# Performance work log

Measured on AMD Instinct MI355X. Metric: run time of the kernel, lower is better.

Reference implementation:

```python
import jax, jax.numpy as jnp
import numpy as np

N_NODES = 50000
N_EDGES = 1600000
IN_FEAT = 256
HIDDEN = 128
N_CLASSES = 16


def gcn_conv(x, edge_index, W, b, n_nodes):
    """PyG GCNConv: x' = D^{-1/2} (A+I) D^{-1/2} (x @ W) + b."""
    h = x @ W  # project first (PyG order), messages are in out_dim
    src, dst = edge_index[0], edge_index[1]
    loops = jnp.arange(n_nodes, dtype=src.dtype)
    src = jnp.concatenate([src, loops])
    dst = jnp.concatenate([dst, loops])
    # degree of A+I (count incoming edges incl. self loop)
    deg = jax.ops.segment_sum(jnp.ones_like(dst, dtype=h.dtype), dst, num_segments=n_nodes)
    dis = jax.lax.rsqrt(deg)  # deg >= 1 thanks to self loops
    norm = dis[src] * dis[dst]  # [E+N]
    msgs = h[src] * norm[:, None]  # gather + scale
    out = jax.ops.segment_sum(msgs, dst, num_segments=n_nodes)  # scatter-add
    return out + b


def setup_inputs() -> dict:
    key = jax.random.key(0)
    k_x, k_e, k_w1, k_b1, k_w2, k_b2 = jax.random.split(key, 6)
    x = jax.random.normal(k_x, (N_NODES, IN_FEAT), dtype=jnp.float32)
    edge_index = jax.random.randint(k_e, (2, N_EDGES), 0, N_NODES, dtype=jnp.int64)
    s1 = 1.0 / np.sqrt(IN_FEAT)
    s2 = 1.0 / np.sqrt(HIDDEN)
    W1 = jax.random.uniform(k_w1, (IN_FEAT, HIDDEN), jnp.float32, -s1, s1)
    b1 = jax.random.uniform(k_b1, (HIDDEN,), jnp.float32, -s1, s1)
    W2 = jax.random.uniform(k_w2, (HIDDEN, N_CLASSES), jnp.float32, -s2, s2)
    b2 = jax.random.uniform(k_b2, (N_CLASSES,), jnp.float32, -s2, s2)
    return {"x": x, "edge_index": edge_index, "W1": W1, "b1": b1, "W2": W2, "b2": b2}


def reference(x, edge_index, W1, b1, W2, b2):
    n = x.shape[0]
    h = gcn_conv(x, edge_index, W1, b1, n)
    h = jax.nn.relu(h)
    logits = gcn_conv(h, edge_index, W2, b2, n)
    return logits, jax.nn.softmax(logits, axis=1)
```

## Files before the change

### kernel.cpp

```cpp
#include <hip/hip_runtime.h>
#include <hip/hip_bf16.h>
#include <math.h>

#define N_NODES 50000
#define N_EDGES 1600000
#define IN_FEAT 256
#define HIDDEN 128
#define N_CLASSES 16

#define ECHUNK 8192
#define NCHK 196
#define NBKT 196
#define BCAP 10240

typedef __attribute__((ext_vector_type(8))) short short8;
typedef __attribute__((ext_vector_type(4))) float floatx4;

__device__ __forceinline__ unsigned short f2bf(float f) {
    unsigned u = __float_as_uint(f);
    return (unsigned short)((u + 0x7fffu + ((u >> 16) & 1u)) >> 16);
}

__device__ __forceinline__ unsigned pk2bf(float a, float b) {
    __hip_bfloat162 h = __float22bfloat162_rn(make_float2(a, b));
    union { __hip_bfloat162 h; unsigned u; } cv;
    cv.h = h;
    return cv.u;
}

__device__ __forceinline__ float bflo(unsigned u) { return __uint_as_float(u << 16); }
__device__ __forceinline__ float bfhi(unsigned u) { return __uint_as_float(u & 0xffff0000u); }

__global__ __launch_bounds__(256) void scatter_edges2(const int* __restrict__ src,
                                                      const int* __restrict__ dst,
                                                      int* __restrict__ cursor,
                                                      unsigned int* __restrict__ sorted,
                                                      const float* __restrict__ W1,
                                                      unsigned short* __restrict__ w1t) {
    __shared__ int hloc[256];
    int t = threadIdx.x;
    hloc[t] = 0;
    if (blockIdx.x < HIDDEN)
        w1t[blockIdx.x * IN_FEAT + t] = f2bf(W1[t * HIDDEN + blockIdx.x]);
    __syncthreads();
    int base = blockIdx.x * ECHUNK;
    int end = min(base + ECHUNK, N_EDGES);
    for (int i = base + t; i < end; i += 256)
        atomicAdd(&hloc[dst[i] >> 8], 1);
    __syncthreads();
    int cnt = hloc[t];
    int lbase = t * BCAP + atomicAdd(&cursor[t], cnt);
    __syncthreads();
    hloc[t] = lbase;
    __syncthreads();
    for (int i = base + t; i < end; i += 256) {
        int d = dst[i];
        int s = src[i];
        int pos = atomicAdd(&hloc[d >> 8], 1);
        sorted[pos] = ((unsigned)d << 16) | (unsigned)s;
    }
}

__global__ __launch_bounds__(256) void build_csr2(const unsigned int* __restrict__ sorted,
                                                  const int* __restrict__ cursor,
                                                  int* __restrict__ rs,
                                                  int* __restrict__ re,
                                                  float* __restrict__ dis,
                                                  unsigned short* __restrict__ csr_src) {
    __shared__ int cnt[256];
    __shared__ int roff[256];
    int t = threadIdx.x;
    int bkt = blockIdx.x;
    int ebase = bkt * BCAP;
    int eend = ebase + cursor[bkt];
    cnt[t] = 0;
    __syncthreads();
    for (int i = ebase + t; i < eend; i += 256)
        atomicAdd(&cnt[(sorted[i] >> 16) & 255], 1);
    __syncthreads();
    int v = cnt[t];
    roff[t] = v;
    __syncthreads();
    for (int off = 1; off < 256; off <<= 1) {
        int x = (t >= off) ? roff[t - off] : 0;
        __syncthreads();
        roff[t] += x;
        __syncthreads();
    }
    int excl = roff[t] - v;
    int node = bkt * 256 + t;
    if (node < N_NODES) {
        rs[node] = ebase + excl;
        re[node] = ebase + excl + v;
        dis[node] = 1.0f / sqrtf((float)(v + 1));
    }
    __syncthreads();
    cnt[t] = ebase + excl;
    __syncthreads();
    for (int i = ebase + t; i < eend; i += 256) {
        unsigned e = sorted[i];
        int pos = atomicAdd(&cnt[(e >> 16) & 255], 1);
        csr_src[pos] = (unsigned short)(e & 0xffffu);
    }
}

#define XCH 260

__global__ __launch_bounds__(256) void gemm1_mfma(const float* __restrict__ x,
                                                  const unsigned short* __restrict__ w1t,
                                                  const float* __restrict__ dis,
                                                  unsigned int* __restrict__ g1) {
    __shared__ float xs[2][8 * XCH];
    int tid = threadIdx.x;
    int w = tid >> 6;
    int lane = tid & 63;
    int quad = lane >> 4;
    int c = lane & 15;
    int row_base = blockIdx.x * 64;
    int wrow = (w >> 1) * 32;
    int col_base = (w & 1) * 64;

    int st_row = min(row_base + 16 * w + (lane >> 3), N_NODES - 1);
    int st_row2 = min(row_base + 16 * w + 8 + (lane >> 3), N_NODES - 1);
    const float* gp1 = x + (size_t)st_row * IN_FEAT + (lane & 7) * 4;
    const float* gp2 = x + (size_t)st_row2 * IN_FEAT + (lane & 7) * 4;

    floatx4 acc[2][4] = {};
    const unsigned short* bp[4];
#pragma unroll
    for (int nt = 0; nt < 4; ++nt)
        bp[nt] = w1t + (size_t)(col_base + nt * 16 + c) * IN_FEAT + quad * 8;

    int dwoff[2];
#pragma unroll
    for (int rt = 0; rt < 2; ++rt) {
        int rit = wrow + rt * 16 + c;
        dwoff[rt] = (rit >> 3) * XCH + (rit & 7) * 32 + quad * 8;
    }

#define STAGE(buf, k0)                                                                  \
    do {                                                                                \
        __builtin_amdgcn_global_load_lds(                                               \
            (const __attribute__((address_space(1))) void*)(gp1 + (k0)),                \
            (__attribute__((address_space(3))) void*)&xs[buf][(2 * w) * XCH], 16, 0, 0);\
        __builtin_amdgcn_global_load_lds(                                               \
            (const __attribute__((address_space(1))) void*)(gp2 + (k0)),                \
            (__attribute__((address_space(3))) void*)&xs[buf][(2 * w + 1) * XCH], 16, 0, 0);\
    } while (0)

    STAGE(0, 0);
    __syncthreads();

    int buf = 0;
#pragma unroll
    for (int kk = 0; kk < 8; ++kk) {
        if (kk < 7) STAGE(buf ^ 1, (kk + 1) * 32);
        short8 b[4];
#pragma unroll
        for (int nt = 0; nt < 4; ++nt)
            b[nt] = *(const short8*)(bp[nt] + kk * 32);
        short8 a[2];
#pragma unroll
        for (int rt = 0; rt < 2; ++rt) {
            float4 f0 = *(const float4*)&xs[buf][dwoff[rt]];
            float4 f1 = *(const float4*)&xs[buf][dwoff[rt] + 4];
            union { short8 s; unsigned u[4]; } au;
            au.u[0] = pk2bf(f0.x, f0.y);
            au.u[1] = pk2bf(f0.z, f0.w);
            au.u[2] = pk2bf(f1.x, f1.y);
            au.u[3] = pk2bf(f1.z, f1.w);
            a[rt] = au.s;
        }
#pragma unroll
        for (int rt = 0; rt < 2; ++rt)
#pragma unroll
            for (int nt = 0; nt < 4; ++nt)
                acc[rt][nt] = __builtin_amdgcn_mfma_f32_16x16x32_bf16(a[rt], b[nt], acc[rt][nt], 0, 0, 0);
        __syncthreads();
        buf ^= 1;
    }
#undef STAGE

    bool evenlane = (lane & 1) == 0;
#pragma unroll
    for (int rt = 0; rt < 2; ++rt) {
#pragma unroll
        for (int reg = 0; reg < 4; ++reg) {
            int row = row_base + wrow + rt * 16 + quad * 4 + reg;
            float dv = dis[min(row, N_NODES - 1)];
#pragma unroll
            for (int nt = 0; nt < 4; ++nt) {
                float v = acc[rt][nt][reg] * dv;
                float vo = __shfl_xor(v, 1);
                if (evenlane && row < N_NODES) {
                    unsigned pkd = (unsigned)f2bf(v) | ((unsigned)f2bf(vo) << 16);
                    g1[(size_t)row * 64 + (col_base >> 1) + nt * 8 + (c >> 1)] = pkd;
                }
            }
        }
    }
}

__global__ __launch_bounds__(256) void agg1_gemm2(const unsigned int* __restrict__ g1,
                                                  const int* __restrict__ rs,
                                                  const int* __restrict__ re,
                                                  const unsigned short* __restrict__ csr_src,
                                                  const float* __restrict__ dis,
                                                  const float* __restrict__ b1,
                                                  const float* __restrict__ W2,
                                                  float* __restrict__ g2) {
    __shared__ float w2s[HIDDEN * N_CLASSES];
    __shared__ float rsh[4][HIDDEN];
    int tid = threadIdx.x;
    for (int i = tid; i < HIDDEN * N_CLASSES; i += 256) w2s[i] = W2[i];
    __syncthreads();

    int wave = tid >> 6;
    int lane = tid & 63;
    int hi = lane >> 5;
    int m = lane & 31;
    int node = blockIdx.x * 4 + wave;
    const uint2* g = (const uint2*)g1;

    float s0 = 0.f, s1 = 0.f, s2 = 0.f, s3 = 0.f;
    float t0 = 0.f, t1 = 0.f, t2 = 0.f, t3 = 0.f;
    if (hi == 0) {
        uint2 su = g[(size_t)node * 32 + m];
        s0 = bflo(su.x); s1 = bfhi(su.x); s2 = bflo(su.y); s3 = bfhi(su.y);
    }

    int e0 = rs[node], e1 = re[node];
    int e = e0;
    for (; e + 16 <= e1; e += 16) {
        int i0 = csr_src[e + 0 + hi], i1 = csr_src[e + 2 + hi];
        int i2 = csr_src[e + 4 + hi], i3 = csr_src[e + 6 + hi];
        int i4 = csr_src[e + 8 + hi], i5 = csr_src[e + 10 + hi];
        int i6 = csr_src[e + 12 + hi], i7 = csr_src[e + 14 + hi];
        uint2 u0 = g[(size_t)i0 * 32 + m];
        uint2 u1 = g[(size_t)i1 * 32 + m];
        uint2 u2 = g[(size_t)i2 * 32 + m];
        uint2 u3 = g[(size_t)i3 * 32 + m];
        uint2 u4 = g[(size_t)i4 * 32 + m];
        uint2 u5 = g[(size_t)i5 * 32 + m];
        uint2 u6 = g[(size_t)i6 * 32 + m];
        uint2 u7 = g[(size_t)i7 * 32 + m];
        s0 += bflo(u0.x); s1 += bfhi(u0.x); s2 += bflo(u0.y); s3 += bfhi(u0.y);
        t0 += bflo(u1.x); t1 += bfhi(u1.x); t2 += bflo(u1.y); t3 += bfhi(u1.y);
        s0 += bflo(u2.x); s1 += bfhi(u2.x); s2 += bflo(u2.y); s3 += bfhi(u2.y);
        t0 += bflo(u3.x); t1 += bfhi(u3.x); t2 += bflo(u3.y); t3 += bfhi(u3.y);
        s0 += bflo(u4.x); s1 += bfhi(u4.x); s2 += bflo(u4.y); s3 += bfhi(u4.y);
        t0 += bflo(u5.x); t1 += bfhi(u5.x); t2 += bflo(u5.y); t3 += bfhi(u5.y);
        s0 += bflo(u6.x); s1 += bfhi(u6.x); s2 += bflo(u6.y); s3 += bfhi(u6.y);
        t0 += bflo(u7.x); t1 += bfhi(u7.x); t2 += bflo(u7.y); t3 += bfhi(u7.y);
    }
    for (; e + 2 <= e1; e += 2) {
        int i0 = csr_src[e + hi];
        uint2 u = g[(size_t)i0 * 32 + m];
        s0 += bflo(u.x); s1 += bfhi(u.x); s2 += bflo(u.y); s3 += bfhi(u.y);
    }
    if (e < e1 && hi == 0) {
        int i0 = csr_src[e];
        uint2 u = g[(size_t)i0 * 32 + m];
        s0 += bflo(u.x); s1 += bfhi(u.x); s2 += bflo(u.y); s3 += bfhi(u.y);
    }
    s0 += t0; s1 += t1; s2 += t2; s3 += t3;
    s0 += __shfl_xor(s0, 32);
    s1 += __shfl_xor(s1, 32);
    s2 += __shfl_xor(s2, 32);
    s3 += __shfl_xor(s3, 32);

    float dv = dis[node];
    if (hi == 0) {
        float4 bb = *(const float4*)&b1[4 * m];
        float4 r;
        r.x = fmaxf(fmaf(dv, s0, bb.x), 0.f);
        r.y = fmaxf(fmaf(dv, s1, bb.y), 0.f);
        r.z = fmaxf(fmaf(dv, s2, bb.z), 0.f);
        r.w = fmaxf(fmaf(dv, s3, bb.w), 0.f);
        *(float4*)&rsh[wave][4 * m] = r;
    }

    int grp = lane >> 4;
    int c = lane & 15;
    int f0 = grp * 32;
    float p = 0.f;
#pragma unroll
    for (int k = 0; k < 32; ++k)
        p = fmaf(rsh[wave][f0 + k], w2s[(f0 + k) * N_CLASSES + c], p);
    p += __shfl_xor(p, 16);
    p += __shfl_xor(p, 32);
    if (lane < 16) g2[(size_t)node * N_CLASSES + lane] = dv * p;
}

__global__ __launch_bounds__(256) void agg2_softmax(const float* __restrict__ g2,
                                                    const int* __restrict__ rs,
                                                    const int* __restrict__ re,
                                                    const unsigned short* __restrict__ csr_src,
                                                    const float* __restrict__ dis,
                                                    const float* __restrict__ b2,
                                                    float* __restrict__ out) {
    int tid = threadIdx.x;
    int node = blockIdx.x * 16 + (tid >> 4);
    int c = tid & 15;
    float acc0 = g2[(size_t)node * N_CLASSES + c];
    float acc1 = 0.f, acc2 = 0.f, acc3 = 0.f;
    float acc4 = 0.f, acc5 = 0.f, acc6 = 0.f, acc7 = 0.f;
    int e0 = rs[node], e1 = re[node];
    int e = e0;
    for (; e + 8 <= e1; e += 8) {
        int s0 = csr_src[e + 0], s1 = csr_src[e + 1], s2 = csr_src[e + 2], s3 = csr_src[e + 3];
        int s4 = csr_src[e + 4], s5 = csr_src[e + 5], s6 = csr_src[e + 6], s7 = csr_src[e + 7];
        acc0 += g2[(size_t)s0 * N_CLASSES + c];
        acc1 += g2[(size_t)s1 * N_CLASSES + c];
        acc2 += g2[(size_t)s2 * N_CLASSES + c];
        acc3 += g2[(size_t)s3 * N_CLASSES + c];
        acc4 += g2[(size_t)s4 * N_CLASSES + c];
        acc5 += g2[(size_t)s5 * N_CLASSES + c];
        acc6 += g2[(size_t)s6 * N_CLASSES + c];
        acc7 += g2[(size_t)s7 * N_CLASSES + c];
    }
    for (; e < e1; ++e) {
        int s = csr_src[e];
        acc0 += g2[(size_t)s * N_CLASSES + c];
    }
    acc0 = ((acc0 + acc1) + (acc2 + acc3)) + ((acc4 + acc5) + (acc6 + acc7));
    float logit = fmaf(dis[node], acc0, b2[c]);
    out[(size_t)node * N_CLASSES + c] = logit;
    float m = logit;
    for (int off = 8; off; off >>= 1) m = fmaxf(m, __shfl_xor(m, off));
    float ex = expf(logit - m);
    float s = ex;
    for (int off = 8; off; off >>= 1) s += __shfl_xor(s, off);
    out[(size_t)N_NODES * N_CLASSES + (size_t)node * N_CLASSES + c] = ex / s;
}


extern "C" void kernel_launch(void* const* d_in, const int* in_sizes, int n_in,
                              void* d_out, int out_size, void* d_ws, size_t ws_size,
                              hipStream_t stream) {
    const float* x  = (const float*)d_in[0];
    const int*   ei = (const int*)d_in[1];
    const float* W1 = (const float*)d_in[2];
    const float* b1 = (const float*)d_in[3];
    const float* W2 = (const float*)d_in[4];
    const float* b2 = (const float*)d_in[5];
    float* out = (float*)d_out;

    char* ws = (char*)d_ws;
    size_t off = 0;
    auto alloc = [&](size_t bytes) -> char* {
        char* p = ws + off;
        off = (off + bytes + 511) & ~(size_t)511;
        return p;
    };
    int*   cursor   = (int*)alloc(256 * 4);
    float* dis      = (float*)alloc(N_NODES * 4);
    int*   rs       = (int*)alloc(N_NODES * 4);
    int*   re       = (int*)alloc(N_NODES * 4);
    unsigned short* w1t = (unsigned short*)alloc((size_t)HIDDEN * IN_FEAT * 2);
    unsigned short* csr_src = (unsigned short*)alloc((size_t)NBKT * BCAP * 2);
    unsigned int* g1 = (unsigned int*)alloc((size_t)N_NODES * 64 * 4);
    float* g2       = (float*)alloc((size_t)N_NODES * N_CLASSES * 4);
    unsigned int* sorted = (unsigned int*)g1;
    (void)ws_size; (void)in_sizes; (void)n_in; (void)out_size;

    const int* src = ei;
    const int* dst = ei + N_EDGES;

    hipMemsetAsync(cursor, 0, 256 * 4, stream);
    scatter_edges2<<<NCHK, 256, 0, stream>>>(src, dst, cursor, sorted, W1, w1t);
    build_csr2<<<NBKT, 256, 0, stream>>>(sorted, cursor, rs, re, dis, csr_src);

    gemm1_mfma<<<(N_NODES + 63) / 64, 256, 0, stream>>>(x, w1t, dis, g1);
    agg1_gemm2<<<N_NODES / 4, 256, 0, stream>>>(g1, rs, re, csr_src, dis, b1, W2, g2);
    agg2_softmax<<<N_NODES / 16, 256, 0, stream>>>(g2, rs, re, csr_src, dis, b2, out);
}
```

Measured before the change: 239.7 us.

## Split hidden features into four planes and map slices to XCDs for aggregation

The first GEMM now writes its bf16 output as four feature-slice planes of 32 columns each, instead of one interleaved row. Each aggregation block handles one slice for 64 nodes. Block indices are mapped so that a given slice stays on the same pair of XCDs, which keeps each plane's gather working set smaller and more cache-resident. Each slice produces a partial second-layer projection, and a new reduce kernel sums the four partials and applies the degree scaling. The cost is one extra launch, four times the partial-buffer traffic, and each slice re-reading the CSR indices.

```diff
diff --git a/kernel.cpp b/kernel.cpp
--- a/kernel.cpp
+++ b/kernel.cpp
@@ -194,102 +194,131 @@
                 float vo = __shfl_xor(v, 1);
                 if (evenlane && row < N_NODES) {
                     unsigned pkd = (unsigned)f2bf(v) | ((unsigned)f2bf(vo) << 16);
-                    g1[(size_t)row * 64 + (col_base >> 1) + nt * 8 + (c >> 1)] = pkd;
+                    int col = col_base + nt * 16 + c;
+                    g1[(size_t)(col >> 5) * (N_NODES * 16) + (size_t)row * 16 + ((col & 31) >> 1)] = pkd;
                 }
             }
         }
     }
 }
 
-__global__ __launch_bounds__(256) void agg1_gemm2(const unsigned int* __restrict__ g1,
-                                                  const int* __restrict__ rs,
-                                                  const int* __restrict__ re,
-                                                  const unsigned short* __restrict__ csr_src,
-                                                  const float* __restrict__ dis,
-                                                  const float* __restrict__ b1,
-                                                  const float* __restrict__ W2,
-                                                  float* __restrict__ g2) {
-    __shared__ float w2s[HIDDEN * N_CLASSES];
-    __shared__ float rsh[4][HIDDEN];
+__global__ __launch_bounds__(256) void agg1_sliced(const uint2* __restrict__ g1,
+                                                   const int* __restrict__ rs,
+                                                   const int* __restrict__ re,
+                                                   const unsigned short* __restrict__ csr_src,
+                                                   const float* __restrict__ dis,
+                                                   const float* __restrict__ b1,
+                                                   const float* __restrict__ W2,
+                                                   float* __restrict__ g2p) {
+    __shared__ float w2s[32 * 16];
+    __shared__ float rbuf[4][8][36];
     int tid = threadIdx.x;
-    for (int i = tid; i < HIDDEN * N_CLASSES; i += 256) w2s[i] = W2[i];
-    __syncthreads();
-
-    int wave = tid >> 6;
-    int lane = tid & 63;
-    int hi = lane >> 5;
-    int m = lane & 31;
-    int node = blockIdx.x * 4 + wave;
-    const uint2* g = (const uint2*)g1;
-
-    float s0 = 0.f, s1 = 0.f, s2 = 0.f, s3 = 0.f;
-    float t0 = 0.f, t1 = 0.f, t2 = 0.f, t3 = 0.f;
-    if (hi == 0) {
-        uint2 su = g[(size_t)node * 32 + m];
-        s0 = bflo(su.x); s1 = bfhi(su.x); s2 = bflo(su.y); s3 = bfhi(su.y);
-    }
-
-    int e0 = rs[node], e1 = re[node];
-    int e = e0;
-    for (; e + 16 <= e1; e += 16) {
-        int i0 = csr_src[e + 0 + hi], i1 = csr_src[e + 2 + hi];
-        int i2 = csr_src[e + 4 + hi], i3 = csr_src[e + 6 + hi];
-        int i4 = csr_src[e + 8 + hi], i5 = csr_src[e + 10 + hi];
-        int i6 = csr_src[e + 12 + hi], i7 = csr_src[e + 14 + hi];
-        uint2 u0 = g[(size_t)i0 * 32 + m];
-        uint2 u1 = g[(size_t)i1 * 32 + m];
-        uint2 u2 = g[(size_t)i2 * 32 + m];
-        uint2 u3 = g[(size_t)i3 * 32 + m];
-        uint2 u4 = g[(size_t)i4 * 32 + m];
-        uint2 u5 = g[(size_t)i5 * 32 + m];
-        uint2 u6 = g[(size_t)i6 * 32 + m];
-        uint2 u7 = g[(size_t)i7 * 32 + m];
-        s0 += bflo(u0.x); s1 += bfhi(u0.x); s2 += bflo(u0.y); s3 += bfhi(u0.y);
-        t0 += bflo(u1.x); t1 += bfhi(u1.x); t2 += bflo(u1.y); t3 += bfhi(u1.y);
-        s0 += bflo(u2.x); s1 += bfhi(u2.x); s2 += bflo(u2.y); s3 += bfhi(u2.y);
-        t0 += bflo(u3.x); t1 += bfhi(u3.x); t2 += bflo(u3.y); t3 += bfhi(u3.y);
-        s0 += bflo(u4.x); s1 += bfhi(u4.x); s2 += bflo(u4.y); s3 += bfhi(u4.y);
-        t0 += bflo(u5.x); t1 += bfhi(u5.x); t2 += bflo(u5.y); t3 += bfhi(u5.y);
-        s0 += bflo(u6.x); s1 += bfhi(u6.x); s2 += bflo(u6.y); s3 += bfhi(u6.y);
-        t0 += bflo(u7.x); t1 += bfhi(u7.x); t2 += bflo(u7.y); t3 += bfhi(u7.y);
-    }
-    for (; e + 2 <= e1; e += 2) {
-        int i0 = csr_src[e + hi];
-        uint2 u = g[(size_t)i0 * 32 + m];
-        s0 += bflo(u.x); s1 += bfhi(u.x); s2 += bflo(u.y); s3 += bfhi(u.y);
-    }
-    if (e < e1 && hi == 0) {
-        int i0 = csr_src[e];
-        uint2 u = g[(size_t)i0 * 32 + m];
-        s0 += bflo(u.x); s1 += bfhi(u.x); s2 += bflo(u.y); s3 += bfhi(u.y);
-    }
-    s0 += t0; s1 += t1; s2 += t2; s3 += t3;
-    s0 += __shfl_xor(s0, 32);
-    s1 += __shfl_xor(s1, 32);
-    s2 += __shfl_xor(s2, 32);
-    s3 += __shfl_xor(s3, 32);
-
-    float dv = dis[node];
-    if (hi == 0) {
-        float4 bb = *(const float4*)&b1[4 * m];
+    int bi = blockIdx.x;
+    int bucket = bi >> 4;
+    int xcd = bi & 7;
+    int slice = xcd >> 1;
+    int quarter = ((bi >> 3) & 1) * 2 + (xcd & 1);
+
+    for (int i = tid; i < 512; i += 256) w2s[i] = W2[slice * 512 + i];
+    __syncthreads();
+
+    int wave = tid >> 6, lane = tid & 63;
+    int g = lane >> 3, m = lane & 7;
+    const uint2* plane = g1 + (size_t)slice * (N_NODES * 8);
+    float* gp = g2p + (size_t)slice * ((size_t)N_NODES * 16);
+    int nbase = bucket * 256 + quarter * 64 + (wave * 8 + g) * 2;
+
+#pragma unroll 1
+    for (int nn = 0; nn < 2; ++nn) {
+        int node = nbase + nn;
+        if (node >= N_NODES) continue;
+        uint2 su = plane[(size_t)node * 8 + m];
+        float s0 = bflo(su.x), s1 = bfhi(su.x), s2 = bflo(su.y), s3 = bfhi(su.y);
+        int e = rs[node], e1v = re[node];
+        for (; e + 8 <= e1v; e += 8) {
+            int i0 = csr_src[e + 0], i1 = csr_src[e + 1];
+            int i2 = csr_src[e + 2], i3 = csr_src[e + 3];
+            int i4 = csr_src[e + 4], i5 = csr_src[e + 5];
+            int i6 = csr_src[e + 6], i7 = csr_src[e + 7];
+            uint2 u0 = plane[(size_t)i0 * 8 + m];
+            uint2 u1 = plane[(size_t)i1 * 8 + m];
+            uint2 u2 = plane[(size_t)i2 * 8 + m];
+            uint2 u3 = plane[(size_t)i3 * 8 + m];
+            uint2 u4 = plane[(size_t)i4 * 8 + m];
+            uint2 u5 = plane[(size_t)i5 * 8 + m];
+            uint2 u6 = plane[(size_t)i6 * 8 + m];
+            uint2 u7 = plane[(size_t)i7 * 8 + m];
+            s0 += bflo(u0.x); s1 += bfhi(u0.x); s2 += bflo(u0.y); s3 += bfhi(u0.y);
+            s0 += bflo(u1.x); s1 += bfhi(u1.x); s2 += bflo(u1.y); s3 += bfhi(u1.y);
+            s0 += bflo(u2.x); s1 += bfhi(u2.x); s2 += bflo(u2.y); s3 += bfhi(u2.y);
+            s0 += bflo(u3.x); s1 += bfhi(u3.x); s2 += bflo(u3.y); s3 += bfhi(u3.y);
+            s0 += bflo(u4.x); s1 += bfhi(u4.x); s2 += bflo(u4.y); s3 += bfhi(u4.y);
+            s0 += bflo(u5.x); s1 += bfhi(u5.x); s2 += bflo(u5.y); s3 += bfhi(u5.y);
+            s0 += bflo(u6.x); s1 += bfhi(u6.x); s2 += bflo(u6.y); s3 += bfhi(u6.y);
+            s0 += bflo(u7.x); s1 += bfhi(u7.x); s2 += bflo(u7.y); s3 += bfhi(u7.y);
+        }
+        if (e < e1v) {
+            int last = e1v - 1;
+            int i0 = csr_src[e];
+            int i1 = csr_src[min(e + 1, last)];
+            int i2 = csr_src[min(e + 2, last)];
+            int i3 = csr_src[min(e + 3, last)];
+            int i4 = csr_src[min(e + 4, last)];
+            int i5 = csr_src[min(e + 5, last)];
+            int i6 = csr_src[min(e + 6, last)];
+            uint2 u0 = plane[(size_t)i0 * 8 + m];
+            uint2 u1 = plane[(size_t)i1 * 8 + m];
+            uint2 u2 = plane[(size_t)i2 * 8 + m];
+            uint2 u3 = plane[(size_t)i3 * 8 + m];
+            uint2 u4 = plane[(size_t)i4 * 8 + m];
+            uint2 u5 = plane[(size_t)i5 * 8 + m];
+            uint2 u6 = plane[(size_t)i6 * 8 + m];
+            s0 += bflo(u0.x); s1 += bfhi(u0.x); s2 += bflo(u0.y); s3 += bfhi(u0.y);
+            if (e + 1 < e1v) { s0 += bflo(u1.x); s1 += bfhi(u1.x); s2 += bflo(u1.y); s3 += bfhi(u1.y); }
+            if (e + 2 < e1v) { s0 += bflo(u2.x); s1 += bfhi(u2.x); s2 += bflo(u2.y); s3 += bfhi(u2.y); }
+            if (e + 3 < e1v) { s0 += bflo(u3.x); s1 += bfhi(u3.x); s2 += bflo(u3.y); s3 += bfhi(u3.y); }
+            if (e + 4 < e1v) { s0 += bflo(u4.x); s1 += bfhi(u4.x); s2 += bflo(u4.y); s3 += bfhi(u4.y); }
+            if (e + 5 < e1v) { s0 += bflo(u5.x); s1 += bfhi(u5.x); s2 += bflo(u5.y); s3 += bfhi(u5.y); }
+            if (e + 6 < e1v) { s0 += bflo(u6.x); s1 += bfhi(u6.x); s2 += bflo(u6.y); s3 += bfhi(u6.y); }
+        }
+        float dv = dis[node];
+        float4 bb = *(const float4*)&b1[slice * 32 + 4 * m];
         float4 r;
         r.x = fmaxf(fmaf(dv, s0, bb.x), 0.f);
         r.y = fmaxf(fmaf(dv, s1, bb.y), 0.f);
         r.z = fmaxf(fmaf(dv, s2, bb.z), 0.f);
         r.w = fmaxf(fmaf(dv, s3, bb.w), 0.f);
-        *(float4*)&rsh[wave][4 * m] = r;
-    }
-
-    int grp = lane >> 4;
-    int c = lane & 15;
-    int f0 = grp * 32;
-    float p = 0.f;
-#pragma unroll
-    for (int k = 0; k < 32; ++k)
-        p = fmaf(rsh[wave][f0 + k], w2s[(f0 + k) * N_CLASSES + c], p);
-    p += __shfl_xor(p, 16);
-    p += __shfl_xor(p, 32);
-    if (lane < 16) g2[(size_t)node * N_CLASSES + lane] = dv * p;
+        *(float4*)&rbuf[wave][g][4 * m] = r;
+        __builtin_amdgcn_sched_barrier(0);
+        float p0 = 0.f, p1 = 0.f;
+#pragma unroll
+        for (int f = 0; f < 32; ++f) {
+            float rv = rbuf[wave][g][f];
+            p0 = fmaf(rv, w2s[f * 16 + 2 * m], p0);
+            p1 = fmaf(rv, w2s[f * 16 + 2 * m + 1], p1);
+        }
+        __builtin_amdgcn_sched_barrier(0);
+        *(float2*)&gp[(size_t)node * 16 + 2 * m] = make_float2(p0, p1);
+    }
+}
+
+__global__ __launch_bounds__(256) void g2_reduce(float* __restrict__ g2p,
+                                                 const float* __restrict__ dis) {
+    int i = blockIdx.x * 256 + threadIdx.x;
+    if (i >= N_NODES * 4) return;
+    const size_t PS = (size_t)N_NODES * 16 / 4;
+    const float4* p = (const float4*)g2p;
+    float4 a = p[i];
+    float4 b = p[i + PS];
+    float4 c = p[i + 2 * PS];
+    float4 d = p[i + 3 * PS];
+    float dv = dis[i >> 2];
+    float4 r;
+    r.x = dv * ((a.x + b.x) + (c.x + d.x));
+    r.y = dv * ((a.y + b.y) + (c.y + d.y));
+    r.z = dv * ((a.z + b.z) + (c.z + d.z));
+    r.w = dv * ((a.w + b.w) + (c.w + d.w));
+    ((float4*)g2p)[i] = r;
 }
 
 __global__ __launch_bounds__(256) void agg2_softmax(const float* __restrict__ g2,
@@ -360,7 +389,7 @@
     unsigned short* w1t = (unsigned short*)alloc((size_t)HIDDEN * IN_FEAT * 2);
     unsigned short* csr_src = (unsigned short*)alloc((size_t)NBKT * BCAP * 2);
     unsigned int* g1 = (unsigned int*)alloc((size_t)N_NODES * 64 * 4);
-    float* g2       = (float*)alloc((size_t)N_NODES * N_CLASSES * 4);
+    float* g2p      = (float*)alloc(4 * (size_t)N_NODES * N_CLASSES * 4);
     unsigned int* sorted = (unsigned int*)g1;
     (void)ws_size; (void)in_sizes; (void)n_in; (void)out_size;
 
@@ -372,6 +401,7 @@
     build_csr2<<<NBKT, 256, 0, stream>>>(sorted, cursor, rs, re, dis, csr_src);
 
     gemm1_mfma<<<(N_NODES + 63) / 64, 256, 0, stream>>>(x, w1t, dis, g1);
-    agg1_gemm2<<<N_NODES / 4, 256, 0, stream>>>(g1, rs, re, csr_src, dis, b1, W2, g2);
-    agg2_softmax<<<N_NODES / 16, 256, 0, stream>>>(g2, rs, re, csr_src, dis, b2, out);
-}
+    agg1_sliced<<<NBKT * 16, 256, 0, stream>>>((const uint2*)g1, rs, re, csr_src, dis, b1, W2, g2p);
+    g2_reduce<<<(N_NODES * 4 + 255) / 256, 256, 0, stream>>>(g2p, dis);
+    agg2_softmax<<<N_NODES / 16, 256, 0, stream>>>(g2p, rs, re, csr_src, dis, b2, out);
+}
```

New measurement: 235.3 us. Within noise of the previous version (-1.8%).
